# Performance work log

Measured on AMD Instinct MI355X. Metric: run time of the kernel, lower is better.

Reference implementation:

```python
import jax, jax.numpy as jnp
import numpy as np


def setup_inputs() -> dict:
    key = jax.random.key(0)
    kq, kk, kv = jax.random.split(key, 3)
    B, S, D = 4, 4096, 64
    return {
        "q": jax.random.normal(kq, (B, S, D), dtype=jnp.float32),
        "k": jax.random.normal(kk, (B, S, D), dtype=jnp.float32),
        "v": jax.random.normal(kv, (B, S, D), dtype=jnp.float32),
    }


def reference(q, k, v):
    B, S, D = q.shape
    scale = 1.0 / jnp.sqrt(jnp.asarray(D, dtype=q.dtype))
    # (B, S, S) full score matrix, as in the naive torch implementation
    scores = jnp.einsum("bqd,bkd->bqk", q, k) * scale
    causal_mask = jnp.tril(jnp.ones((S, S), dtype=bool))  # True = keep
    scores = jnp.where(causal_mask, scores, -jnp.inf)
    attn = jax.nn.softmax(scores, axis=-1)
    return jnp.einsum("bqk,bkd->bqd", attn, v)
```

## Files before the change

### kernel.cpp

```cpp
#include <hip/hip_runtime.h>
#include <hip/hip_bf16.h>

typedef __bf16 bf16x8 __attribute__((ext_vector_type(8)));
typedef __bf16 bf16x4 __attribute__((ext_vector_type(4)));
typedef float  floatx4 __attribute__((ext_vector_type(4)));

#define SD 4096
#define DH 64
#define NB 4

__device__ __forceinline__ float exp2fast(float x) { return __builtin_amdgcn_exp2f(x); }

__device__ __forceinline__ unsigned pack_bf16_2(float a, float b) {
    union { __bf16 h[2]; unsigned u; } cvt;
    cvt.h[0] = (__bf16)a; cvt.h[1] = (__bf16)b;
    return cvt.u;
}

__device__ __forceinline__ void block_sync_lds() {
    asm volatile("s_waitcnt lgkmcnt(0)\n\ts_barrier" ::: "memory");
}

__global__ __launch_bounds__(256) void prep_kernel(const float* __restrict__ v,
                                                   __bf16* __restrict__ vt) {
    __shared__ __bf16 tile[16][80];
    const int bid = blockIdx.x;
    const int tid = threadIdx.x;
    const int b = bid >> 8, kt = (bid >> 2) & 63, dq = bid & 3;
    {
        int key = tid >> 2, ds = (tid & 3) * 4;
        float4 f = *(const float4*)(v + ((long)b * SD + kt * 64 + key) * DH + dq * 16 + ds);
        tile[ds+0][key] = (__bf16)f.x;
        tile[ds+1][key] = (__bf16)f.y;
        tile[ds+2][key] = (__bf16)f.z;
        tile[ds+3][key] = (__bf16)f.w;
    }
    __syncthreads();
    {
        int dloc = tid >> 4, cs = (tid & 15) * 4;
        bf16x4 o;
#pragma unroll
        for (int i = 0; i < 4; ++i) {
            int col = cs + i;
            int key = ((col >> 5) * 2 + ((col >> 2) & 1)) * 16
                    + ((col >> 3) & 3) * 4 + (col & 3);
            o[i] = tile[dloc][key];
        }
        *(bf16x4*)(vt + ((long)b * DH + dq * 16 + dloc) * SD + kt * 64 + cs) = o;
    }
}

__global__ __launch_bounds__(256, 2) void fa_kernel(const float* __restrict__ q,
                                                    const float* __restrict__ kq,
                                                    const __bf16* __restrict__ vt,
                                                    __bf16* __restrict__ opart,
                                                    float* __restrict__ lpart) {
    __shared__ __bf16 smem[2][8192];

    const int tid  = threadIdx.x;
    const int wave = tid >> 6;
    const int lane = tid & 63;
    const int c    = lane & 15;
    const int quad = lane >> 4;
    const int bid   = blockIdx.x;
    const int batch = bid & 3;
    const int pr    = (bid >> 2) & 15;
    const int qr    = bid >> 6;
    const float sc = 0.125f * 1.4426950408889634f;

    const long offB   = (long)batch * SD * DH;
    const long vtoffB = (long)batch * DH * SD;

    const int krow = tid >> 2, kdc = (tid & 3) * 16;
    auto swz = [](int g) { int row = g >> 3, ch = g & 7; return row * 64 + ((ch ^ (row & 7)) << 3); };
    const int wkA = swz(krow * 8 + (tid & 3) * 2);
    const int wkB = swz(krow * 8 + (tid & 3) * 2 + 1);
    const int gk0 = tid, gk1 = tid + 256;
    const int wv0 = 4096 + swz(gk0), wv1 = 4096 + swz(gk1);
    const int sw   = c & 7;
    const int off0 = ((quad ^ sw) << 3);
    const int off1 = (((quad + 4) ^ sw) << 3);
    const int rowc = c * 64;

#pragma unroll 1
    for (int ph = 0; ph < 2; ++ph) {
        const int T = ph ? 31 - pr : pr;
        const int myq = T * 128 + wave * 32;

        bf16x8 qf0A, qf1A, qf0B, qf1B;
#pragma unroll
        for (int h = 0; h < 2; ++h) {
            const float* qp = q + offB + (long)(myq + h*16 + c) * DH + quad * 8;
            float4 f0 = *(const float4*)(qp);
            float4 f1 = *(const float4*)(qp + 4);
            float4 f2 = *(const float4*)(qp + 32);
            float4 f3 = *(const float4*)(qp + 36);
            bf16x8 t0, t1;
            t0[0]=(__bf16)(f0.x*sc); t0[1]=(__bf16)(f0.y*sc); t0[2]=(__bf16)(f0.z*sc); t0[3]=(__bf16)(f0.w*sc);
            t0[4]=(__bf16)(f1.x*sc); t0[5]=(__bf16)(f1.y*sc); t0[6]=(__bf16)(f1.z*sc); t0[7]=(__bf16)(f1.w*sc);
            t1[0]=(__bf16)(f2.x*sc); t1[1]=(__bf16)(f2.y*sc); t1[2]=(__bf16)(f2.z*sc); t1[3]=(__bf16)(f2.w*sc);
            t1[4]=(__bf16)(f3.x*sc); t1[5]=(__bf16)(f3.y*sc); t1[6]=(__bf16)(f3.z*sc); t1[7]=(__bf16)(f3.w*sc);
            if (h == 0) { qf0A = t0; qf1A = t1; } else { qf0B = t0; qf1B = t1; }
        }

        floatx4 oA0 = {0.f,0.f,0.f,0.f}, oA1 = oA0, oA2 = oA0, oA3 = oA0;
        floatx4 oB0 = oA0, oB1 = oA0, oB2 = oA0, oB3 = oA0;
        float lA = 0.0f, lB = 0.0f;

        const int kmax = 2 * T + 1;
        const int n = (kmax >= qr) ? ((kmax - qr) >> 3) + 1 : 0;

        float4 fk0, fk1, fk2, fk3;
        bf16x8 sv0, sv1;
        auto stage = [&](int kt, float4& a0, float4& a1, float4& a2, float4& a3,
                         bf16x8& v0, bf16x8& v1) {
            const float* kg = kq + offB + (long)(kt * 64 + krow) * DH + kdc;
            a0 = *(const float4*)(kg);
            a1 = *(const float4*)(kg + 4);
            a2 = *(const float4*)(kg + 8);
            a3 = *(const float4*)(kg + 12);
            const __bf16* vg = vt + vtoffB + kt * 64;
            v0 = *(const bf16x8*)(vg + (long)(gk0 >> 3) * SD + (gk0 & 7) * 8);
            v1 = *(const bf16x8*)(vg + (long)(gk1 >> 3) * SD + (gk1 & 7) * 8);
        };

        if (n > 0) stage(qr, fk0, fk1, fk2, fk3, sv0, sv1);
        block_sync_lds();

#pragma unroll 1
        for (int j = 0; j < n; ++j) {
            const int kt = qr + 8 * j;
            float4 nk0, nk1, nk2, nk3; bf16x8 nv0, nv1;
            if (j + 1 < n) stage(kt + 8, nk0, nk1, nk2, nk3, nv0, nv1);
            __bf16* buf = smem[j & 1];
            {
                bf16x8 cA, cB;
                cA[0]=(__bf16)fk0.x; cA[1]=(__bf16)fk0.y; cA[2]=(__bf16)fk0.z; cA[3]=(__bf16)fk0.w;
                cA[4]=(__bf16)fk1.x; cA[5]=(__bf16)fk1.y; cA[6]=(__bf16)fk1.z; cA[7]=(__bf16)fk1.w;
                cB[0]=(__bf16)fk2.x; cB[1]=(__bf16)fk2.y; cB[2]=(__bf16)fk2.z; cB[3]=(__bf16)fk2.w;
                cB[4]=(__bf16)fk3.x; cB[5]=(__bf16)fk3.y; cB[6]=(__bf16)fk3.z; cB[7]=(__bf16)fk3.w;
                *(bf16x8*)(buf + wkA) = cA;
                *(bf16x8*)(buf + wkB) = cB;
                *(bf16x8*)(buf + wv0) = sv0;
                *(bf16x8*)(buf + wv1) = sv1;
            }
            fk0 = nk0; fk1 = nk1; fk2 = nk2; fk3 = nk3; sv0 = nv0; sv1 = nv1;
            block_sync_lds();

            const int kbase = kt * 64;
            if (kbase > myq + 31) continue;

            const __bf16* kbuf = buf;
            const __bf16* vbuf = buf + 4096;
            floatx4 saA[4], saB[4];
#pragma unroll
            for (int t = 0; t < 4; ++t) {
                bf16x8 ka  = *(const bf16x8*)(kbuf + t * 1024 + rowc + off0);
                bf16x8 kb2 = *(const bf16x8*)(kbuf + t * 1024 + rowc + off1);
                floatx4 a = {0.f,0.f,0.f,0.f}, b = a;
                a = __builtin_amdgcn_mfma_f32_16x16x32_bf16(ka,  qf0A, a, 0, 0, 0);
                a = __builtin_amdgcn_mfma_f32_16x16x32_bf16(kb2, qf1A, a, 0, 0, 0);
                b = __builtin_amdgcn_mfma_f32_16x16x32_bf16(ka,  qf0B, b, 0, 0, 0);
                b = __builtin_amdgcn_mfma_f32_16x16x32_bf16(kb2, qf1B, b, 0, 0, 0);
                saA[t] = a; saB[t] = b;
            }
            float peA[16], peB[16];
            if (kbase + 63 > myq) {
                const int qrA = myq + c, qrB = myq + 16 + c;
#pragma unroll
                for (int t = 0; t < 4; ++t)
#pragma unroll
                    for (int r = 0; r < 4; ++r) {
                        int key = kbase + t*16 + quad*4 + r;
                        peA[t*4+r] = (key <= qrA) ? exp2fast(saA[t][r]) : 0.0f;
                        peB[t*4+r] = (key <= qrB) ? exp2fast(saB[t][r]) : 0.0f;
                    }
            } else {
#pragma unroll
                for (int t = 0; t < 4; ++t)
#pragma unroll
                    for (int r = 0; r < 4; ++r) {
                        peA[t*4+r] = exp2fast(saA[t][r]);
                        peB[t*4+r] = exp2fast(saB[t][r]);
                    }
            }
            {
                float s8[8], s4v[4];
#pragma unroll
                for (int i = 0; i < 8; ++i) s8[i] = peA[i] + peA[i+8];
#pragma unroll
                for (int i = 0; i < 4; ++i) s4v[i] = s8[i] + s8[i+4];
                lA += (s4v[0] + s4v[2]) + (s4v[1] + s4v[3]);
#pragma unroll
                for (int i = 0; i < 8; ++i) s8[i] = peB[i] + peB[i+8];
#pragma unroll
                for (int i = 0; i < 4; ++i) s4v[i] = s8[i] + s8[i+4];
                lB += (s4v[0] + s4v[2]) + (s4v[1] + s4v[3]);
            }
#pragma unroll
            for (int s = 0; s < 2; ++s) {
                union { unsigned u[4]; bf16x8 f; } bpA, bpB;
#pragma unroll
                for (int jj = 0; jj < 4; ++jj) {
                    bpA.u[jj] = pack_bf16_2(peA[8*s + 2*jj], peA[8*s + 2*jj + 1]);
                    bpB.u[jj] = pack_bf16_2(peB[8*s + 2*jj], peB[8*s + 2*jj + 1]);
                }
                const int offs = s ? off1 : off0;
                bf16x8 v0 = *(const bf16x8*)(vbuf + 0*1024 + rowc + offs);
                bf16x8 v1 = *(const bf16x8*)(vbuf + 1*1024 + rowc + offs);
                bf16x8 v2 = *(const bf16x8*)(vbuf + 2*1024 + rowc + offs);
                bf16x8 v3 = *(const bf16x8*)(vbuf + 3*1024 + rowc + offs);
                oA0 = __builtin_amdgcn_mfma_f32_16x16x32_bf16(v0, bpA.f, oA0, 0, 0, 0);
                oA1 = __builtin_amdgcn_mfma_f32_16x16x32_bf16(v1, bpA.f, oA1, 0, 0, 0);
                oA2 = __builtin_amdgcn_mfma_f32_16x16x32_bf16(v2, bpA.f, oA2, 0, 0, 0);
                oA3 = __builtin_amdgcn_mfma_f32_16x16x32_bf16(v3, bpA.f, oA3, 0, 0, 0);
                oB0 = __builtin_amdgcn_mfma_f32_16x16x32_bf16(v0, bpB.f, oB0, 0, 0, 0);
                oB1 = __builtin_amdgcn_mfma_f32_16x16x32_bf16(v1, bpB.f, oB1, 0, 0, 0);
                oB2 = __builtin_amdgcn_mfma_f32_16x16x32_bf16(v2, bpB.f, oB2, 0, 0, 0);
                oB3 = __builtin_amdgcn_mfma_f32_16x16x32_bf16(v3, bpB.f, oB3, 0, 0, 0);
            }
        }

        lA += __shfl_xor(lA, 16); lA += __shfl_xor(lA, 32);
        lB += __shfl_xor(lB, 16); lB += __shfl_xor(lB, 32);

        __bf16* ob = opart + ((long)qr * NB + batch) * (long)(SD * DH) + (long)myq * DH;
        {
            floatx4 ovA[4] = {oA0, oA1, oA2, oA3};
            floatx4 ovB[4] = {oB0, oB1, oB2, oB3};
#pragma unroll
            for (int dt = 0; dt < 4; ++dt) {
                uint2 sA, sB;
                sA.x = pack_bf16_2(ovA[dt][0], ovA[dt][1]);
                sA.y = pack_bf16_2(ovA[dt][2], ovA[dt][3]);
                sB.x = pack_bf16_2(ovB[dt][0], ovB[dt][1]);
                sB.y = pack_bf16_2(ovB[dt][2], ovB[dt][3]);
                *(uint2*)(ob + (c)      * DH + dt*16 + quad*4) = sA;
                *(uint2*)(ob + (16 + c) * DH + dt*16 + quad*4) = sB;
            }
        }
        if (quad == 0) {
            lpart[((long)qr * NB + batch) * SD + myq + c]      = lA;
            lpart[((long)qr * NB + batch) * SD + myq + 16 + c] = lB;
        }
    }
}

__global__ __launch_bounds__(256) void combine_kernel(const __bf16* __restrict__ opart,
                                                      const float* __restrict__ lpart,
                                                      float* __restrict__ out) {
    const long t    = (long)blockIdx.x * 256 + threadIdx.x;
    const long base = t * 4;
    const long qq   = base >> 6;
    float n0 = 0.f, n1 = 0.f, n2 = 0.f, n3 = 0.f, den = 0.f;
#pragma unroll
    for (int qr = 0; qr < 8; ++qr) {
        bf16x4 p = *(const bf16x4*)(opart + ((long)qr << 20) + base);
        n0 += (float)p[0]; n1 += (float)p[1]; n2 += (float)p[2]; n3 += (float)p[3];
        den += lpart[((long)qr << 14) + qq];
    }
    float inv = 1.0f / den;
    float4 o; o.x = n0 * inv; o.y = n1 * inv; o.z = n2 * inv; o.w = n3 * inv;
    *(float4*)(out + base) = o;
}

extern "C" void kernel_launch(void* const* d_in, const int* in_sizes, int n_in,
                              void* d_out, int out_size, void* d_ws, size_t ws_size,
                              hipStream_t stream) {
    const float* q = (const float*)d_in[0];
    const float* k = (const float*)d_in[1];
    const float* v = (const float*)d_in[2];
    float* out = (float*)d_out;
    __bf16* vtb   = (__bf16*)d_ws;
    __bf16* opart = (__bf16*)((char*)d_ws + (4u << 20));
    float*  lpart = (float*)((char*)d_ws + (20u << 20));
    prep_kernel<<<dim3(1024), dim3(256), 0, stream>>>(v, vtb);
    fa_kernel<<<dim3(512), dim3(256), 0, stream>>>(q, k, vtb, opart, lpart);
    combine_kernel<<<dim3(1024), dim3(256), 0, stream>>>(opart, lpart, out);
}
```

Baseline: 93.36 us.

## Halve per-wave query rows to 16 and double grid size for occupancy

Each wave now processes 16 query rows instead of 32, and each block covers a 64-row query tile instead of 128. The grid doubles to 1024 blocks and the launch-bounds occupancy hint rises from 2 to 4 blocks per CU. The aim is more parallelism and fewer registers per wave on the 256-CU part. The cost is that each loaded K/V tile is reused across half as many query rows, so LDS traffic and global loads per unit of compute roughly double.

```diff
diff --git a/kernel.cpp b/kernel.cpp
--- a/kernel.cpp
+++ b/kernel.cpp
@@ -50,7 +50,7 @@
     }
 }
 
-__global__ __launch_bounds__(256, 2) void fa_kernel(const float* __restrict__ q,
+__global__ __launch_bounds__(256, 4) void fa_kernel(const float* __restrict__ q,
                                                     const float* __restrict__ kq,
                                                     const __bf16* __restrict__ vt,
                                                     __bf16* __restrict__ opart,
@@ -64,8 +64,8 @@
     const int quad = lane >> 4;
     const int bid   = blockIdx.x;
     const int batch = bid & 3;
-    const int pr    = (bid >> 2) & 15;
-    const int qr    = bid >> 6;
+    const int pr    = (bid >> 2) & 31;
+    const int qr    = bid >> 7;
     const float sc = 0.125f * 1.4426950408889634f;
 
     const long offB   = (long)batch * SD * DH;
@@ -84,31 +84,27 @@
 
 #pragma unroll 1
     for (int ph = 0; ph < 2; ++ph) {
-        const int T = ph ? 31 - pr : pr;
-        const int myq = T * 128 + wave * 32;
-
-        bf16x8 qf0A, qf1A, qf0B, qf1B;
-#pragma unroll
-        for (int h = 0; h < 2; ++h) {
-            const float* qp = q + offB + (long)(myq + h*16 + c) * DH + quad * 8;
+        const int T = ph ? 63 - pr : pr;
+        const int myq = T * 64 + wave * 16;
+        const int qrow = myq + c;
+
+        bf16x8 qf0, qf1;
+        {
+            const float* qp = q + offB + (long)(myq + c) * DH + quad * 8;
             float4 f0 = *(const float4*)(qp);
             float4 f1 = *(const float4*)(qp + 4);
             float4 f2 = *(const float4*)(qp + 32);
             float4 f3 = *(const float4*)(qp + 36);
-            bf16x8 t0, t1;
-            t0[0]=(__bf16)(f0.x*sc); t0[1]=(__bf16)(f0.y*sc); t0[2]=(__bf16)(f0.z*sc); t0[3]=(__bf16)(f0.w*sc);
-            t0[4]=(__bf16)(f1.x*sc); t0[5]=(__bf16)(f1.y*sc); t0[6]=(__bf16)(f1.z*sc); t0[7]=(__bf16)(f1.w*sc);
-            t1[0]=(__bf16)(f2.x*sc); t1[1]=(__bf16)(f2.y*sc); t1[2]=(__bf16)(f2.z*sc); t1[3]=(__bf16)(f2.w*sc);
-            t1[4]=(__bf16)(f3.x*sc); t1[5]=(__bf16)(f3.y*sc); t1[6]=(__bf16)(f3.z*sc); t1[7]=(__bf16)(f3.w*sc);
-            if (h == 0) { qf0A = t0; qf1A = t1; } else { qf0B = t0; qf1B = t1; }
-        }
-
-        floatx4 oA0 = {0.f,0.f,0.f,0.f}, oA1 = oA0, oA2 = oA0, oA3 = oA0;
-        floatx4 oB0 = oA0, oB1 = oA0, oB2 = oA0, oB3 = oA0;
-        float lA = 0.0f, lB = 0.0f;
-
-        const int kmax = 2 * T + 1;
-        const int n = (kmax >= qr) ? ((kmax - qr) >> 3) + 1 : 0;
+            qf0[0]=(__bf16)(f0.x*sc); qf0[1]=(__bf16)(f0.y*sc); qf0[2]=(__bf16)(f0.z*sc); qf0[3]=(__bf16)(f0.w*sc);
+            qf0[4]=(__bf16)(f1.x*sc); qf0[5]=(__bf16)(f1.y*sc); qf0[6]=(__bf16)(f1.z*sc); qf0[7]=(__bf16)(f1.w*sc);
+            qf1[0]=(__bf16)(f2.x*sc); qf1[1]=(__bf16)(f2.y*sc); qf1[2]=(__bf16)(f2.z*sc); qf1[3]=(__bf16)(f2.w*sc);
+            qf1[4]=(__bf16)(f3.x*sc); qf1[5]=(__bf16)(f3.y*sc); qf1[6]=(__bf16)(f3.z*sc); qf1[7]=(__bf16)(f3.w*sc);
+        }
+
+        floatx4 o0 = {0.f,0.f,0.f,0.f}, o1 = o0, o2 = o0, o3 = o0;
+        float l = 0.0f;
+
+        const int n = (T >= qr) ? ((T - qr) >> 3) + 1 : 0;
 
         float4 fk0, fk1, fk2, fk3;
         bf16x8 sv0, sv1;
@@ -148,101 +144,77 @@
             block_sync_lds();
 
             const int kbase = kt * 64;
-            if (kbase > myq + 31) continue;
+            if (kbase > myq + 15) continue;
 
             const __bf16* kbuf = buf;
             const __bf16* vbuf = buf + 4096;
-            floatx4 saA[4], saB[4];
+            floatx4 sa[4];
 #pragma unroll
             for (int t = 0; t < 4; ++t) {
                 bf16x8 ka  = *(const bf16x8*)(kbuf + t * 1024 + rowc + off0);
                 bf16x8 kb2 = *(const bf16x8*)(kbuf + t * 1024 + rowc + off1);
-                floatx4 a = {0.f,0.f,0.f,0.f}, b = a;
-                a = __builtin_amdgcn_mfma_f32_16x16x32_bf16(ka,  qf0A, a, 0, 0, 0);
-                a = __builtin_amdgcn_mfma_f32_16x16x32_bf16(kb2, qf1A, a, 0, 0, 0);
-                b = __builtin_amdgcn_mfma_f32_16x16x32_bf16(ka,  qf0B, b, 0, 0, 0);
-                b = __builtin_amdgcn_mfma_f32_16x16x32_bf16(kb2, qf1B, b, 0, 0, 0);
-                saA[t] = a; saB[t] = b;
-            }
-            float peA[16], peB[16];
+                floatx4 a = {0.f,0.f,0.f,0.f};
+                a = __builtin_amdgcn_mfma_f32_16x16x32_bf16(ka,  qf0, a, 0, 0, 0);
+                a = __builtin_amdgcn_mfma_f32_16x16x32_bf16(kb2, qf1, a, 0, 0, 0);
+                sa[t] = a;
+            }
+            float pe[16];
             if (kbase + 63 > myq) {
-                const int qrA = myq + c, qrB = myq + 16 + c;
 #pragma unroll
                 for (int t = 0; t < 4; ++t)
 #pragma unroll
                     for (int r = 0; r < 4; ++r) {
                         int key = kbase + t*16 + quad*4 + r;
-                        peA[t*4+r] = (key <= qrA) ? exp2fast(saA[t][r]) : 0.0f;
-                        peB[t*4+r] = (key <= qrB) ? exp2fast(saB[t][r]) : 0.0f;
+                        pe[t*4+r] = (key <= qrow) ? exp2fast(sa[t][r]) : 0.0f;
                     }
             } else {
 #pragma unroll
                 for (int t = 0; t < 4; ++t)
 #pragma unroll
-                    for (int r = 0; r < 4; ++r) {
-                        peA[t*4+r] = exp2fast(saA[t][r]);
-                        peB[t*4+r] = exp2fast(saB[t][r]);
-                    }
+                    for (int r = 0; r < 4; ++r) pe[t*4+r] = exp2fast(sa[t][r]);
             }
             {
                 float s8[8], s4v[4];
 #pragma unroll
-                for (int i = 0; i < 8; ++i) s8[i] = peA[i] + peA[i+8];
+                for (int i = 0; i < 8; ++i) s8[i] = pe[i] + pe[i+8];
 #pragma unroll
                 for (int i = 0; i < 4; ++i) s4v[i] = s8[i] + s8[i+4];
-                lA += (s4v[0] + s4v[2]) + (s4v[1] + s4v[3]);
-#pragma unroll
-                for (int i = 0; i < 8; ++i) s8[i] = peB[i] + peB[i+8];
-#pragma unroll
-                for (int i = 0; i < 4; ++i) s4v[i] = s8[i] + s8[i+4];
-                lB += (s4v[0] + s4v[2]) + (s4v[1] + s4v[3]);
+                l += (s4v[0] + s4v[2]) + (s4v[1] + s4v[3]);
             }
 #pragma unroll
             for (int s = 0; s < 2; ++s) {
-                union { unsigned u[4]; bf16x8 f; } bpA, bpB;
-#pragma unroll
-                for (int jj = 0; jj < 4; ++jj) {
-                    bpA.u[jj] = pack_bf16_2(peA[8*s + 2*jj], peA[8*s + 2*jj + 1]);
-                    bpB.u[jj] = pack_bf16_2(peB[8*s + 2*jj], peB[8*s + 2*jj + 1]);
-                }
+                union { unsigned u[4]; bf16x8 f; } bp;
+#pragma unroll
+                for (int jj = 0; jj < 4; ++jj)
+                    bp.u[jj] = pack_bf16_2(pe[8*s + 2*jj], pe[8*s + 2*jj + 1]);
                 const int offs = s ? off1 : off0;
                 bf16x8 v0 = *(const bf16x8*)(vbuf + 0*1024 + rowc + offs);
                 bf16x8 v1 = *(const bf16x8*)(vbuf + 1*1024 + rowc + offs);
                 bf16x8 v2 = *(const bf16x8*)(vbuf + 2*1024 + rowc + offs);
                 bf16x8 v3 = *(const bf16x8*)(vbuf + 3*1024 + rowc + offs);
-                oA0 = __builtin_amdgcn_mfma_f32_16x16x32_bf16(v0, bpA.f, oA0, 0, 0, 0);
-                oA1 = __builtin_amdgcn_mfma_f32_16x16x32_bf16(v1, bpA.f, oA1, 0, 0, 0);
-                oA2 = __builtin_amdgcn_mfma_f32_16x16x32_bf16(v2, bpA.f, oA2, 0, 0, 0);
-                oA3 = __builtin_amdgcn_mfma_f32_16x16x32_bf16(v3, bpA.f, oA3, 0, 0, 0);
-                oB0 = __builtin_amdgcn_mfma_f32_16x16x32_bf16(v0, bpB.f, oB0, 0, 0, 0);
-                oB1 = __builtin_amdgcn_mfma_f32_16x16x32_bf16(v1, bpB.f, oB1, 0, 0, 0);
-                oB2 = __builtin_amdgcn_mfma_f32_16x16x32_bf16(v2, bpB.f, oB2, 0, 0, 0);
-                oB3 = __builtin_amdgcn_mfma_f32_16x16x32_bf16(v3, bpB.f, oB3, 0, 0, 0);
-            }
-        }
-
-        lA += __shfl_xor(lA, 16); lA += __shfl_xor(lA, 32);
-        lB += __shfl_xor(lB, 16); lB += __shfl_xor(lB, 32);
+                o0 = __builtin_amdgcn_mfma_f32_16x16x32_bf16(v0, bp.f, o0, 0, 0, 0);
+                o1 = __builtin_amdgcn_mfma_f32_16x16x32_bf16(v1, bp.f, o1, 0, 0, 0);
+                o2 = __builtin_amdgcn_mfma_f32_16x16x32_bf16(v2, bp.f, o2, 0, 0, 0);
+                o3 = __builtin_amdgcn_mfma_f32_16x16x32_bf16(v3, bp.f, o3, 0, 0, 0);
+            }
+        }
+
+        l += __shfl_xor(l, 16);
+        l += __shfl_xor(l, 32);
 
         __bf16* ob = opart + ((long)qr * NB + batch) * (long)(SD * DH) + (long)myq * DH;
         {
-            floatx4 ovA[4] = {oA0, oA1, oA2, oA3};
-            floatx4 ovB[4] = {oB0, oB1, oB2, oB3};
+            floatx4 ov[4] = {o0, o1, o2, o3};
 #pragma unroll
             for (int dt = 0; dt < 4; ++dt) {
-                uint2 sA, sB;
-                sA.x = pack_bf16_2(ovA[dt][0], ovA[dt][1]);
-                sA.y = pack_bf16_2(ovA[dt][2], ovA[dt][3]);
-                sB.x = pack_bf16_2(ovB[dt][0], ovB[dt][1]);
-                sB.y = pack_bf16_2(ovB[dt][2], ovB[dt][3]);
-                *(uint2*)(ob + (c)      * DH + dt*16 + quad*4) = sA;
-                *(uint2*)(ob + (16 + c) * DH + dt*16 + quad*4) = sB;
-            }
-        }
-        if (quad == 0) {
-            lpart[((long)qr * NB + batch) * SD + myq + c]      = lA;
-            lpart[((long)qr * NB + batch) * SD + myq + 16 + c] = lB;
-        }
+                uint2 sO;
+                sO.x = pack_bf16_2(ov[dt][0], ov[dt][1]);
+                sO.y = pack_bf16_2(ov[dt][2], ov[dt][3]);
+                *(uint2*)(ob + c * DH + dt*16 + quad*4) = sO;
+            }
+        }
+        if (quad == 0)
+            lpart[((long)qr * NB + batch) * SD + myq + c] = l;
     }
 }
 
@@ -275,6 +247,6 @@
     __bf16* opart = (__bf16*)((char*)d_ws + (4u << 20));
     float*  lpart = (float*)((char*)d_ws + (20u << 20));
     prep_kernel<<<dim3(1024), dim3(256), 0, stream>>>(v, vtb);
-    fa_kernel<<<dim3(512), dim3(256), 0, stream>>>(q, k, vtb, opart, lpart);
+    fa_kernel<<<dim3(1024), dim3(256), 0, stream>>>(q, k, vtb, opart, lpart);
     combine_kernel<<<dim3(1024), dim3(256), 0, stream>>>(opart, lpart, out);
 }
```

After: 94.23 us. Within noise of the previous version (+0.9%).
